# Performance work log

Measured on AMD Instinct MI355X. Metric: run time of the kernel, lower is better.

## Reference

```python
import jax, jax.numpy as jnp
import numpy as np

B, T, C = 4, 2048, 1024
H = 16
D = C // H  # head_dim = 64


def setup_inputs() -> dict:
    key = jax.random.key(0)
    k1, k2, k3, k4, k5 = jax.random.split(key, 5)
    s = 1.0 / np.sqrt(C)
    return {
        "hidden_state": jax.random.normal(k1, (B, T, C), dtype=jnp.float32),
        "qkv_w": jax.random.uniform(k2, (C, 3 * C), jnp.float32, -s, s),
        "qkv_b": jax.random.uniform(k3, (3 * C,), jnp.float32, -s, s),
        "o_w": jax.random.uniform(k4, (C, C), jnp.float32, -s, s),
        "o_b": jax.random.uniform(k5, (C,), jnp.float32, -s, s),
    }


def reference(hidden_state, qkv_w, qkv_b, o_w, o_b):
    Bq, Tq, Cq = hidden_state.shape
    qkv = hidden_state @ qkv_w + qkv_b  # [B,T,3C]
    q, k, v = jnp.split(qkv, 3, axis=-1)
    # [B,T,C] -> [B,H,T,D]
    q = q.reshape(Bq, Tq, H, D).transpose(0, 2, 1, 3)
    k = k.reshape(Bq, Tq, H, D).transpose(0, 2, 1, 3)
    v = v.reshape(Bq, Tq, H, D).transpose(0, 2, 1, 3)
    scaling = D ** (-0.5)
    scores = jnp.einsum("bhqd,bhkd->bhqk", q, k) * scaling  # [B,H,T,T]
    causal = jnp.tril(jnp.ones((Tq, Tq), dtype=bool))
    scores = jnp.where(causal[None, None], scores, -jnp.inf)
    attn = jax.nn.softmax(scores, axis=-1)
    out = jnp.einsum("bhqk,bhkd->bhqd", attn, v)  # [B,H,T,D]
    out = out.transpose(0, 2, 1, 3).reshape(Bq, Tq, Cq)
    return out @ o_w + o_b
```

## Files before the change

### kernel.cpp

```cpp
#include <hip/hip_runtime.h>
#include <hip/hip_bf16.h>

#define Bn 4
#define Tn 2048
#define Cn 1024
#define Hn 16
#define Dn 64
#define Kdim 1024

typedef __bf16 bf16x8 __attribute__((ext_vector_type(8)));
typedef float f32x4 __attribute__((ext_vector_type(4)));
union B8 { uint4 u; bf16x8 f; ushort s[8]; };

static __device__ __forceinline__ ushort f2bf(float x) {
    __hip_bfloat16 h = __float2bfloat16(x);
    return *(ushort*)&h;
}

#define AS1 __attribute__((address_space(1)))
#define AS3 __attribute__((address_space(3)))

static __device__ __forceinline__ void gload_lds16(const ushort* g, ushort* l) {
    __builtin_amdgcn_global_load_lds((AS1 const uint4*)(const void*)g,
                                     (AS3 uint4*)(void*)l, 16, 0, 0);
}

__global__ __launch_bounds__(256) void cvt_bf16(
    const float* __restrict__ src, ushort* __restrict__ dst, int n)
{
    int i = (blockIdx.x * 256 + threadIdx.x) * 8;
    if (i >= n) return;
    float4 a = *(const float4*)&src[i];
    float4 b = *(const float4*)&src[i + 4];
    ushort4 o0, o1;
    o0.x = f2bf(a.x); o0.y = f2bf(a.y); o0.z = f2bf(a.z); o0.w = f2bf(a.w);
    o1.x = f2bf(b.x); o1.y = f2bf(b.y); o1.z = f2bf(b.z); o1.w = f2bf(b.w);
    *(ushort4*)&dst[i] = o0;
    *(ushort4*)&dst[i + 4] = o1;
}

__global__ __launch_bounds__(256) void transpose_bf16(
    const float* __restrict__ W, ushort* __restrict__ Wt, int N)
{
    __shared__ float Ls[32][33];
    const int k0 = blockIdx.y * 32, n0 = blockIdx.x * 32;
    const int tx = threadIdx.x & 31, ty = threadIdx.x >> 5;
    #pragma unroll
    for (int i = 0; i < 4; i++) {
        int r = ty + i * 8;
        Ls[r][tx] = W[(size_t)(k0 + r) * N + n0 + tx];
    }
    __syncthreads();
    #pragma unroll
    for (int i = 0; i < 4; i++) {
        int r = ty + i * 8;
        Wt[(size_t)(n0 + r) * Kdim + k0 + tx] = f2bf(Ls[tx][r]);
    }
}

template <int EPI>
__global__ __launch_bounds__(256) void gemm_bt(
    const ushort* __restrict__ A, const ushort* __restrict__ Bt,
    const float* __restrict__ bias,
    float* __restrict__ Out, ushort* __restrict__ Qb,
    ushort* __restrict__ Kb, ushort* __restrict__ Vtb)
{
    const int m0 = blockIdx.y * 128;
    const int n0 = blockIdx.x * 128;
    const int t  = threadIdx.x;
    const int wave = t >> 6, lane = t & 63;
    const int ln = lane & 15, quad = lane >> 4;
    const int wm = wave >> 1, wn = wave & 1;

    __shared__ ushort As[128 * 64];
    __shared__ ushort Bs[128 * 64];

    f32x4 acc[4][4] = {};

    for (int k0 = 0; k0 < Kdim; k0 += 64) {
        __syncthreads();
        #pragma unroll
        for (int it = 0; it < 4; it++) {
            int c = it * 256 + wave * 64 + lane;
            int row = c >> 3, seg = c & 7;
            int gseg = seg ^ (row & 7);
            gload_lds16(&A [(size_t)(m0 + row) * Kdim + k0 + gseg * 8], &As[c * 8]);
            gload_lds16(&Bt[(size_t)(n0 + row) * Kdim + k0 + gseg * 8], &Bs[c * 8]);
        }
        __syncthreads();

        #pragma unroll
        for (int ks = 0; ks < 2; ks++) {
            bf16x8 af[4], bf[4];
            #pragma unroll
            for (int mm = 0; mm < 4; mm++) {
                int row = wm * 64 + mm * 16 + ln;
                int seg = (ks * 4 + quad) ^ (ln & 7);
                B8 tmp; tmp.u = *(const uint4*)&As[row * 64 + seg * 8];
                af[mm] = tmp.f;
            }
            #pragma unroll
            for (int nn = 0; nn < 4; nn++) {
                int row = wn * 64 + nn * 16 + ln;
                int seg = (ks * 4 + quad) ^ (ln & 7);
                B8 tmp; tmp.u = *(const uint4*)&Bs[row * 64 + seg * 8];
                bf[nn] = tmp.f;
            }
            #pragma unroll
            for (int mm = 0; mm < 4; mm++)
                #pragma unroll
                for (int nn = 0; nn < 4; nn++)
                    acc[mm][nn] = __builtin_amdgcn_mfma_f32_16x16x32_bf16(
                        af[mm], bf[nn], acc[mm][nn], 0, 0, 0);
        }
    }

    if (EPI == 0) {
        #pragma unroll
        for (int nn = 0; nn < 4; nn++) {
            int n = n0 + wn * 64 + nn * 16 + ln;
            float bv = bias[n];
            #pragma unroll
            for (int mm = 0; mm < 4; mm++) {
                int mbase = m0 + wm * 64 + mm * 16 + quad * 4;
                #pragma unroll
                for (int reg = 0; reg < 4; reg++)
                    Out[(size_t)(mbase + reg) * 1024 + n] = acc[mm][nn][reg] + bv;
            }
        }
    } else {
        const int nb = n0 + wn * 64;
        const int which = nb >> 10;
        const int h = (nb & 1023) >> 6;
        const float scale = (which == 0) ? 0.125f * 1.44269504088896f : 1.0f;
        #pragma unroll
        for (int nn = 0; nn < 4; nn++) {
            int n = nb + nn * 16 + ln;
            float bv = bias[n];
            #pragma unroll
            for (int mm = 0; mm < 4; mm++) {
                int mbase = m0 + wm * 64 + mm * 16 + quad * 4;
                int b_ = mbase >> 11, tt = mbase & 2047;
                if (which == 2) {
                    ushort4 o;
                    #pragma unroll
                    for (int reg = 0; reg < 4; reg++)
                        ((ushort*)&o)[reg] = f2bf(acc[mm][nn][reg] + bv);
                    *(ushort4*)&Vtb[((size_t)((b_ * Hn + h) * Dn) + nn * 16 + ln) * Tn + tt] = o;
                } else {
                    ushort* dst = (which == 0) ? Qb : Kb;
                    #pragma unroll
                    for (int reg = 0; reg < 4; reg++)
                        dst[((size_t)((b_ * Hn + h) * Tn + tt + reg)) * Dn + nn * 16 + ln] =
                            f2bf((acc[mm][nn][reg] + bv) * scale);
                }
            }
        }
    }
}

__global__ __launch_bounds__(256, 2) void attn_mfma(
    const ushort* __restrict__ Qb, const ushort* __restrict__ Kb,
    const ushort* __restrict__ Vtb, ushort* __restrict__ Ob)
{
    const int pair = blockIdx.x;
    const int bh   = blockIdx.y;
    const int t    = threadIdx.x;
    const int wave = t >> 6, lane = t & 63;
    const int ln   = lane & 15, quad = lane >> 4;

    __shared__ ushort Ks[2][128 * 64];
    __shared__ ushort Ps[4][32 * 66];

    const ushort* KgB = Kb  + (size_t)bh * Tn * Dn;
    const ushort* VgB = Vtb + (size_t)bh * Dn * Tn;
    const int b_ = bh >> 4, h = bh & 15;

    #define STAGE_K(kc, buf)                                                   \
        do {                                                                   \
            _Pragma("unroll")                                                  \
            for (int it = 0; it < 4; it++) {                                   \
                int c = it * 256 + wave * 64 + lane;                           \
                int row = c >> 3, seg = c & 7;                                 \
                int gs = seg ^ (row & 7);                                      \
                gload_lds16(&KgB[(size_t)((kc) * 128 + row) * Dn + gs * 8],    \
                            &Ks[buf][c * 8]);                                  \
            }                                                                  \
        } while (0)

    int cur = 0;
    STAGE_K(0, 0);

    for (int tile = 0; tile < 2; tile++) {
        const int qt = (tile == 0) ? pair : 15 - pair;
        const int q0 = qt * 128;

        const ushort* Qg = Qb + ((size_t)bh * Tn + q0 + wave * 32) * Dn;
        bf16x8 qf[2][2];
        #pragma unroll
        for (int ns = 0; ns < 2; ns++)
            #pragma unroll
            for (int ks = 0; ks < 2; ks++) {
                B8 tmp; tmp.u = *(const uint4*)&Qg[(ns * 16 + ln) * 64 + ks * 32 + quad * 8];
                qf[ns][ks] = tmp.f;
            }

        f32x4 Oacc[4][2] = {};
        float m_r[2] = {-1e30f, -1e30f}, l_r[2] = {0.f, 0.f};

        for (int kc = 0; kc <= qt; kc++) {
            __syncthreads();

            B8 vfr[4][4];
            #pragma unroll
            for (int gks = 0; gks < 4; gks++)
                #pragma unroll
                for (int ctd = 0; ctd < 4; ctd++)
                    vfr[ctd][gks].u = *(const uint4*)&VgB[
                        (size_t)(ctd * 16 + ln) * Tn + kc * 128 + gks * 32 + quad * 8];

            if (kc < qt)            STAGE_K(kc + 1, cur ^ 1);
            else if (tile == 0)     STAGE_K(0, cur ^ 1);

            const ushort* Kc = Ks[cur];
            f32x4 S[8][2] = {};
            #pragma unroll
            for (int ks = 0; ks < 2; ks++)
                #pragma unroll
                for (int ct = 0; ct < 8; ct++) {
                    B8 a; a.u = *(const uint4*)&Kc[(ct * 16 + ln) * 64 +
                                                   (((ks * 4 + quad) ^ (ln & 7)) * 8)];
                    #pragma unroll
                    for (int ns = 0; ns < 2; ns++)
                        S[ct][ns] = __builtin_amdgcn_mfma_f32_16x16x32_bf16(
                            a.f, qf[ns][ks], S[ct][ns], 0, 0, 0);
                }

            if (kc == qt) {
                #pragma unroll
                for (int ct = 0; ct < 8; ct++) {
                    int keyl = ct * 16 + quad * 4;
                    #pragma unroll
                    for (int ns = 0; ns < 2; ns++) {
                        int ql = wave * 32 + ns * 16 + ln;
                        #pragma unroll
                        for (int reg = 0; reg < 4; reg++)
                            if (keyl + reg > ql) S[ct][ns][reg] = -1e30f;
                    }
                }
            }

            float alpha[2], ssum[2] = {0.f, 0.f};
            #pragma unroll
            for (int ns = 0; ns < 2; ns++) {
                float pm = -1e30f;
                #pragma unroll
                for (int ct = 0; ct < 8; ct++)
                    #pragma unroll
                    for (int reg = 0; reg < 4; reg++)
                        pm = fmaxf(pm, S[ct][ns][reg]);
                pm = fmaxf(pm, __shfl_xor(pm, 16));
                pm = fmaxf(pm, __shfl_xor(pm, 32));
                float mn = fmaxf(m_r[ns], pm);
                alpha[ns] = exp2f(m_r[ns] - mn);
                m_r[ns] = mn;
                #pragma unroll
                for (int ctd = 0; ctd < 4; ctd++)
                    Oacc[ctd][ns] *= alpha[ns];
            }

            ushort* Pw = Ps[wave];
            #pragma unroll
            for (int pass = 0; pass < 2; pass++) {
                #pragma unroll
                for (int ct_h = 0; ct_h < 4; ct_h++) {
                    int ct = pass * 4 + ct_h;
                    #pragma unroll
                    for (int ns = 0; ns < 2; ns++) {
                        ushort4 o;
                        #pragma unroll
                        for (int reg = 0; reg < 4; reg++) {
                            float p = exp2f(S[ct][ns][reg] - m_r[ns]);
                            ssum[ns] += p;
                            ((ushort*)&o)[reg] = f2bf(p);
                        }
                        *(ushort4*)&Pw[(ns * 16 + ln) * 66 + ct_h * 16 + quad * 4] = o;
                    }
                }
                #pragma unroll
                for (int kh = 0; kh < 2; kh++) {
                    int gks = pass * 2 + kh;
                    #pragma unroll
                    for (int ns = 0; ns < 2; ns++) {
                        B8 pfr; pfr.u = *(const uint4*)&Pw[(ns * 16 + ln) * 66 +
                                                           kh * 32 + quad * 8];
                        #pragma unroll
                        for (int ctd = 0; ctd < 4; ctd++)
                            Oacc[ctd][ns] = __builtin_amdgcn_mfma_f32_16x16x32_bf16(
                                vfr[ctd][gks].f, pfr.f, Oacc[ctd][ns], 0, 0, 0);
                    }
                }
            }
            #pragma unroll
            for (int ns = 0; ns < 2; ns++) {
                float s = ssum[ns];
                s += __shfl_xor(s, 16);
                s += __shfl_xor(s, 32);
                l_r[ns] = l_r[ns] * alpha[ns] + s;
            }
            cur ^= 1;
        }

        #pragma unroll
        for (int ns = 0; ns < 2; ns++) {
            float inv = 1.0f / l_r[ns];
            int token = q0 + wave * 32 + ns * 16 + ln;
            ushort* dst = Ob + ((size_t)(b_ * Tn + token)) * Cn + h * 64;
            #pragma unroll
            for (int ctd = 0; ctd < 4; ctd++) {
                ushort4 o;
                #pragma unroll
                for (int reg = 0; reg < 4; reg++)
                    ((ushort*)&o)[reg] = f2bf(Oacc[ctd][ns][reg] * inv);
                *(ushort4*)&dst[ctd * 16 + quad * 4] = o;
            }
        }
    }
    #undef STAGE_K
}

extern "C" void kernel_launch(void* const* d_in, const int* in_sizes, int n_in,
                              void* d_out, int out_size, void* d_ws, size_t ws_size,
                              hipStream_t stream) {
    const float* X     = (const float*)d_in[0];
    const float* qkv_w = (const float*)d_in[1];
    const float* qkv_b = (const float*)d_in[2];
    const float* o_w   = (const float*)d_in[3];
    const float* o_b   = (const float*)d_in[4];
    float* out = (float*)d_out;

    const size_t BTC = (size_t)Bn * Tn * Cn;
    ushort* Xb  = (ushort*)d_ws;
    ushort* Wqt = Xb  + BTC;
    ushort* Wot = Wqt + 3 * Cn * Cn;
    ushort* Qb  = Wot + Cn * Cn;
    ushort* Kb  = Qb  + BTC;
    ushort* Vtb = Kb  + BTC;
    ushort* Ao  = Vtb + BTC;

    cvt_bf16<<<dim3((int)(BTC / 8 / 256)), 256, 0, stream>>>(X, Xb, (int)BTC);
    transpose_bf16<<<dim3(3 * Cn / 32, Kdim / 32), 256, 0, stream>>>(qkv_w, Wqt, 3 * Cn);
    transpose_bf16<<<dim3(Cn / 32, Kdim / 32), 256, 0, stream>>>(o_w, Wot, Cn);

    gemm_bt<1><<<dim3(3 * Cn / 128, 8192 / 128), 256, 0, stream>>>(
        Xb, Wqt, qkv_b, nullptr, Qb, Kb, Vtb);
    attn_mfma<<<dim3(8, Bn * Hn), 256, 0, stream>>>(Qb, Kb, Vtb, Ao);
    gemm_bt<0><<<dim3(Cn / 128, 8192 / 128), 256, 0, stream>>>(
        Ao, Wot, o_b, out, nullptr, nullptr, nullptr);
}
```

Before: 313.4 us.

## Stage QKV epilogue through LDS for coalesced stores; one query tile per attention block

The QKV GEMM epilogue now writes bias-added bf16 results into a swizzled LDS tile (reusing the As/Bs buffers) and then emits 16-byte coalesced global stores for Q, K and the transposed V, replacing scattered 2-byte and 8-byte strided stores. The attention kernel drops the paired-tile scheme, in which each block handled a short and a long query tile. Each block now handles a single query tile, with blocks ordered so that longer tiles launch first, and the grid doubles to 16 blocks per head. This raises parallelism but relies on the hardware scheduler rather than explicit pairing to balance the triangular causal workload.

Result: slower. 412.8 us (+31.7%).

```diff
diff --git a/kernel.cpp b/kernel.cpp
--- a/kernel.cpp
+++ b/kernel.cpp
@@ -133,27 +133,56 @@
         const int which = nb >> 10;
         const int h = (nb & 1023) >> 6;
         const float scale = (which == 0) ? 0.125f * 1.44269504088896f : 1.0f;
-        #pragma unroll
-        for (int nn = 0; nn < 4; nn++) {
-            int n = nb + nn * 16 + ln;
-            float bv = bias[n];
-            #pragma unroll
-            for (int mm = 0; mm < 4; mm++) {
-                int mbase = m0 + wm * 64 + mm * 16 + quad * 4;
-                int b_ = mbase >> 11, tt = mbase & 2047;
-                if (which == 2) {
-                    ushort4 o;
-                    #pragma unroll
-                    for (int reg = 0; reg < 4; reg++)
-                        ((ushort*)&o)[reg] = f2bf(acc[mm][nn][reg] + bv);
-                    *(ushort4*)&Vtb[((size_t)((b_ * Hn + h) * Dn) + nn * 16 + ln) * Tn + tt] = o;
-                } else {
-                    ushort* dst = (which == 0) ? Qb : Kb;
-                    #pragma unroll
-                    for (int reg = 0; reg < 4; reg++)
-                        dst[((size_t)((b_ * Hn + h) * Tn + tt + reg)) * Dn + nn * 16 + ln] =
+        const int b_ = m0 >> 11;
+        const int t0 = (m0 & 2047) + wm * 64;
+
+        __syncthreads();
+        ushort* tile = ((wave & 2) ? Bs : As) + (wave & 1) * 4096;
+
+        if (which == 2) {
+            #pragma unroll
+            for (int nn = 0; nn < 4; nn++) {
+                float bv = bias[nb + nn * 16 + ln];
+                #pragma unroll
+                for (int mm = 0; mm < 4; mm++)
+                    #pragma unroll
+                    for (int reg = 0; reg < 4; reg++) {
+                        int m = mm * 16 + quad * 4 + reg;
+                        int n = nn * 16 + ln;
+                        tile[n * 64 + (m ^ (((n >> 1) & 7) * 8))] =
+                            f2bf(acc[mm][nn][reg] + bv);
+                    }
+            }
+            #pragma unroll
+            for (int it = 0; it < 8; it++) {
+                int idx = it * 64 + lane;
+                int row = idx >> 3, seg = idx & 7;
+                uint4 v = *(const uint4*)&tile[row * 64 +
+                              ((seg * 8) ^ (((row >> 1) & 7) * 8))];
+                *(uint4*)&Vtb[((size_t)((b_ * Hn + h) * Dn) + row) * Tn + t0 + seg * 8] = v;
+            }
+        } else {
+            ushort* dst = (which == 0) ? Qb : Kb;
+            #pragma unroll
+            for (int nn = 0; nn < 4; nn++) {
+                float bv = bias[nb + nn * 16 + ln];
+                #pragma unroll
+                for (int mm = 0; mm < 4; mm++)
+                    #pragma unroll
+                    for (int reg = 0; reg < 4; reg++) {
+                        int m = mm * 16 + quad * 4 + reg;
+                        int n = nn * 16 + ln;
+                        tile[m * 64 + (n ^ (((m >> 1) & 7) * 8))] =
                             f2bf((acc[mm][nn][reg] + bv) * scale);
-                }
+                    }
+            }
+            #pragma unroll
+            for (int it = 0; it < 8; it++) {
+                int idx = it * 64 + lane;
+                int row = idx >> 3, seg = idx & 7;
+                uint4 v = *(const uint4*)&tile[row * 64 +
+                              ((seg * 8) ^ (((row >> 1) & 7) * 8))];
+                *(uint4*)&dst[((size_t)((b_ * Hn + h) * Tn) + t0 + row) * Dn + seg * 8] = v;
             }
         }
     }
@@ -163,7 +192,7 @@
     const ushort* __restrict__ Qb, const ushort* __restrict__ Kb,
     const ushort* __restrict__ Vtb, ushort* __restrict__ Ob)
 {
-    const int pair = blockIdx.x;
+    const int qt   = 15 - blockIdx.x;
     const int bh   = blockIdx.y;
     const int t    = threadIdx.x;
     const int wave = t >> 6, lane = t & 63;
@@ -191,139 +220,135 @@
     int cur = 0;
     STAGE_K(0, 0);
 
-    for (int tile = 0; tile < 2; tile++) {
-        const int qt = (tile == 0) ? pair : 15 - pair;
-        const int q0 = qt * 128;
-
-        const ushort* Qg = Qb + ((size_t)bh * Tn + q0 + wave * 32) * Dn;
-        bf16x8 qf[2][2];
-        #pragma unroll
-        for (int ns = 0; ns < 2; ns++)
-            #pragma unroll
-            for (int ks = 0; ks < 2; ks++) {
-                B8 tmp; tmp.u = *(const uint4*)&Qg[(ns * 16 + ln) * 64 + ks * 32 + quad * 8];
-                qf[ns][ks] = tmp.f;
-            }
-
-        f32x4 Oacc[4][2] = {};
-        float m_r[2] = {-1e30f, -1e30f}, l_r[2] = {0.f, 0.f};
-
-        for (int kc = 0; kc <= qt; kc++) {
-            __syncthreads();
-
-            B8 vfr[4][4];
-            #pragma unroll
-            for (int gks = 0; gks < 4; gks++)
-                #pragma unroll
-                for (int ctd = 0; ctd < 4; ctd++)
-                    vfr[ctd][gks].u = *(const uint4*)&VgB[
-                        (size_t)(ctd * 16 + ln) * Tn + kc * 128 + gks * 32 + quad * 8];
-
-            if (kc < qt)            STAGE_K(kc + 1, cur ^ 1);
-            else if (tile == 0)     STAGE_K(0, cur ^ 1);
-
-            const ushort* Kc = Ks[cur];
-            f32x4 S[8][2] = {};
-            #pragma unroll
-            for (int ks = 0; ks < 2; ks++)
-                #pragma unroll
-                for (int ct = 0; ct < 8; ct++) {
-                    B8 a; a.u = *(const uint4*)&Kc[(ct * 16 + ln) * 64 +
-                                                   (((ks * 4 + quad) ^ (ln & 7)) * 8)];
-                    #pragma unroll
-                    for (int ns = 0; ns < 2; ns++)
-                        S[ct][ns] = __builtin_amdgcn_mfma_f32_16x16x32_bf16(
-                            a.f, qf[ns][ks], S[ct][ns], 0, 0, 0);
+    const int q0 = qt * 128;
+
+    const ushort* Qg = Qb + ((size_t)bh * Tn + q0 + wave * 32) * Dn;
+    bf16x8 qf[2][2];
+    #pragma unroll
+    for (int ns = 0; ns < 2; ns++)
+        #pragma unroll
+        for (int ks = 0; ks < 2; ks++) {
+            B8 tmp; tmp.u = *(const uint4*)&Qg[(ns * 16 + ln) * 64 + ks * 32 + quad * 8];
+            qf[ns][ks] = tmp.f;
+        }
+
+    f32x4 Oacc[4][2] = {};
+    float m_r[2] = {-1e30f, -1e30f}, l_r[2] = {0.f, 0.f};
+
+    for (int kc = 0; kc <= qt; kc++) {
+        __syncthreads();
+
+        B8 vfr[4][4];
+        #pragma unroll
+        for (int gks = 0; gks < 4; gks++)
+            #pragma unroll
+            for (int ctd = 0; ctd < 4; ctd++)
+                vfr[ctd][gks].u = *(const uint4*)&VgB[
+                    (size_t)(ctd * 16 + ln) * Tn + kc * 128 + gks * 32 + quad * 8];
+
+        if (kc < qt) STAGE_K(kc + 1, cur ^ 1);
+
+        const ushort* Kc = Ks[cur];
+        f32x4 S[8][2] = {};
+        #pragma unroll
+        for (int ks = 0; ks < 2; ks++)
+            #pragma unroll
+            for (int ct = 0; ct < 8; ct++) {
+                B8 a; a.u = *(const uint4*)&Kc[(ct * 16 + ln) * 64 +
+                                               (((ks * 4 + quad) ^ (ln & 7)) * 8)];
+                #pragma unroll
+                for (int ns = 0; ns < 2; ns++)
+                    S[ct][ns] = __builtin_amdgcn_mfma_f32_16x16x32_bf16(
+                        a.f, qf[ns][ks], S[ct][ns], 0, 0, 0);
+            }
+
+        if (kc == qt) {
+            #pragma unroll
+            for (int ct = 0; ct < 8; ct++) {
+                int keyl = ct * 16 + quad * 4;
+                #pragma unroll
+                for (int ns = 0; ns < 2; ns++) {
+                    int ql = wave * 32 + ns * 16 + ln;
+                    #pragma unroll
+                    for (int reg = 0; reg < 4; reg++)
+                        if (keyl + reg > ql) S[ct][ns][reg] = -1e30f;
                 }
-
-            if (kc == qt) {
-                #pragma unroll
-                for (int ct = 0; ct < 8; ct++) {
-                    int keyl = ct * 16 + quad * 4;
-                    #pragma unroll
-                    for (int ns = 0; ns < 2; ns++) {
-                        int ql = wave * 32 + ns * 16 + ln;
-                        #pragma unroll
-                        for (int reg = 0; reg < 4; reg++)
-                            if (keyl + reg > ql) S[ct][ns][reg] = -1e30f;
+            }
+        }
+
+        float alpha[2], ssum[2] = {0.f, 0.f};
+        #pragma unroll
+        for (int ns = 0; ns < 2; ns++) {
+            float pm = -1e30f;
+            #pragma unroll
+            for (int ct = 0; ct < 8; ct++)
+                #pragma unroll
+                for (int reg = 0; reg < 4; reg++)
+                    pm = fmaxf(pm, S[ct][ns][reg]);
+            pm = fmaxf(pm, __shfl_xor(pm, 16));
+            pm = fmaxf(pm, __shfl_xor(pm, 32));
+            float mn = fmaxf(m_r[ns], pm);
+            alpha[ns] = exp2f(m_r[ns] - mn);
+            m_r[ns] = mn;
+            #pragma unroll
+            for (int ctd = 0; ctd < 4; ctd++)
+                Oacc[ctd][ns] *= alpha[ns];
+        }
+
+        ushort* Pw = Ps[wave];
+        #pragma unroll
+        for (int pass = 0; pass < 2; pass++) {
+            #pragma unroll
+            for (int ct_h = 0; ct_h < 4; ct_h++) {
+                int ct = pass * 4 + ct_h;
+                #pragma unroll
+                for (int ns = 0; ns < 2; ns++) {
+                    ushort4 o;
+                    #pragma unroll
+                    for (int reg = 0; reg < 4; reg++) {
+                        float p = exp2f(S[ct][ns][reg] - m_r[ns]);
+                        ssum[ns] += p;
+                        ((ushort*)&o)[reg] = f2bf(p);
                     }
+                    *(ushort4*)&Pw[(ns * 16 + ln) * 66 + ct_h * 16 + quad * 4] = o;
                 }
             }
-
-            float alpha[2], ssum[2] = {0.f, 0.f};
-            #pragma unroll
-            for (int ns = 0; ns < 2; ns++) {
-                float pm = -1e30f;
-                #pragma unroll
-                for (int ct = 0; ct < 8; ct++)
-                    #pragma unroll
-                    for (int reg = 0; reg < 4; reg++)
-                        pm = fmaxf(pm, S[ct][ns][reg]);
-                pm = fmaxf(pm, __shfl_xor(pm, 16));
-                pm = fmaxf(pm, __shfl_xor(pm, 32));
-                float mn = fmaxf(m_r[ns], pm);
-                alpha[ns] = exp2f(m_r[ns] - mn);
-                m_r[ns] = mn;
-                #pragma unroll
-                for (int ctd = 0; ctd < 4; ctd++)
-                    Oacc[ctd][ns] *= alpha[ns];
-            }
-
-            ushort* Pw = Ps[wave];
-            #pragma unroll
-            for (int pass = 0; pass < 2; pass++) {
-                #pragma unroll
-                for (int ct_h = 0; ct_h < 4; ct_h++) {
-                    int ct = pass * 4 + ct_h;
-                    #pragma unroll
-                    for (int ns = 0; ns < 2; ns++) {
-                        ushort4 o;
-                        #pragma unroll
-                        for (int reg = 0; reg < 4; reg++) {
-                            float p = exp2f(S[ct][ns][reg] - m_r[ns]);
-                            ssum[ns] += p;
-                            ((ushort*)&o)[reg] = f2bf(p);
-                        }
-                        *(ushort4*)&Pw[(ns * 16 + ln) * 66 + ct_h * 16 + quad * 4] = o;
-                    }
+            #pragma unroll
+            for (int kh = 0; kh < 2; kh++) {
+                int gks = pass * 2 + kh;
+                #pragma unroll
+                for (int ns = 0; ns < 2; ns++) {
+                    B8 pfr; pfr.u = *(const uint4*)&Pw[(ns * 16 + ln) * 66 +
+                                                       kh * 32 + quad * 8];
+                    #pragma unroll
+                    for (int ctd = 0; ctd < 4; ctd++)
+                        Oacc[ctd][ns] = __builtin_amdgcn_mfma_f32_16x16x32_bf16(
+                            vfr[ctd][gks].f, pfr.f, Oacc[ctd][ns], 0, 0, 0);
                 }
-                #pragma unroll
-                for (int kh = 0; kh < 2; kh++) {
-                    int gks = pass * 2 + kh;
-                    #pragma unroll
-                    for (int ns = 0; ns < 2; ns++) {
-                        B8 pfr; pfr.u = *(const uint4*)&Pw[(ns * 16 + ln) * 66 +
-                                                           kh * 32 + quad * 8];
-                        #pragma unroll
-                        for (int ctd = 0; ctd < 4; ctd++)
-                            Oacc[ctd][ns] = __builtin_amdgcn_mfma_f32_16x16x32_bf16(
-                                vfr[ctd][gks].f, pfr.f, Oacc[ctd][ns], 0, 0, 0);
-                    }
-                }
-            }
-            #pragma unroll
-            for (int ns = 0; ns < 2; ns++) {
-                float s = ssum[ns];
-                s += __shfl_xor(s, 16);
-                s += __shfl_xor(s, 32);
-                l_r[ns] = l_r[ns] * alpha[ns] + s;
-            }
-            cur ^= 1;
-        }
-
+            }
+        }
         #pragma unroll
         for (int ns = 0; ns < 2; ns++) {
-            float inv = 1.0f / l_r[ns];
-            int token = q0 + wave * 32 + ns * 16 + ln;
-            ushort* dst = Ob + ((size_t)(b_ * Tn + token)) * Cn + h * 64;
-            #pragma unroll
-            for (int ctd = 0; ctd < 4; ctd++) {
-                ushort4 o;
-                #pragma unroll
-                for (int reg = 0; reg < 4; reg++)
-                    ((ushort*)&o)[reg] = f2bf(Oacc[ctd][ns][reg] * inv);
-                *(ushort4*)&dst[ctd * 16 + quad * 4] = o;
-            }
+            float s = ssum[ns];
+            s += __shfl_xor(s, 16);
+            s += __shfl_xor(s, 32);
+            l_r[ns] = l_r[ns] * alpha[ns] + s;
+        }
+        cur ^= 1;
+    }
+
+    #pragma unroll
+    for (int ns = 0; ns < 2; ns++) {
+        float inv = 1.0f / l_r[ns];
+        int token = q0 + wave * 32 + ns * 16 + ln;
+        ushort* dst = Ob + ((size_t)(b_ * Tn + token)) * Cn + h * 64;
+        #pragma unroll
+        for (int ctd = 0; ctd < 4; ctd++) {
+            ushort4 o;
+            #pragma unroll
+            for (int reg = 0; reg < 4; reg++)
+                ((ushort*)&o)[reg] = f2bf(Oacc[ctd][ns][reg] * inv);
+            *(ushort4*)&dst[ctd * 16 + quad * 4] = o;
         }
     }
     #undef STAGE_K
@@ -354,7 +379,7 @@
 
     gemm_bt<1><<<dim3(3 * Cn / 128, 8192 / 128), 256, 0, stream>>>(
         Xb, Wqt, qkv_b, nullptr, Qb, Kb, Vtb);
-    attn_mfma<<<dim3(8, Bn * Hn), 256, 0, stream>>>(Qb, Kb, Vtb, Ao);
+    attn_mfma<<<dim3(16, Bn * Hn), 256, 0, stream>>>(Qb, Kb, Vtb, Ao);
     gemm_bt<0><<<dim3(Cn / 128, 8192 / 128), 256, 0, stream>>>(
         Ao, Wot, o_b, out, nullptr, nullptr, nullptr);
 }
```
